# Kernel optimization log

Hardware: AMD Instinct MI355X
Metric: run time of the kernel (lower is better)

Reference implementation:

```python
import jax, jax.numpy as jnp
import numpy as np

N, D, H = 1024, 256, 256


def setup_inputs() -> dict:
    key = jax.random.key(0)
    k1, k2, k3, k4, k5 = jax.random.split(key, 5)
    z = jax.random.normal(k1, (N, D), dtype=jnp.float32)
    # fc1: Linear(2*D, H) -> weight [H, 2*D], bias [H]
    lim1 = 1.0 / np.sqrt(2 * D)
    W1 = jax.random.uniform(k2, (H, 2 * D), dtype=jnp.float32, minval=-lim1, maxval=lim1)
    b1 = jax.random.uniform(k3, (H,), dtype=jnp.float32, minval=-lim1, maxval=lim1)
    # fc2: Linear(H, 1)
    lim2 = 1.0 / np.sqrt(H)
    W2 = jax.random.uniform(k4, (1, H), dtype=jnp.float32, minval=-lim2, maxval=lim2)
    b2 = jax.random.uniform(k5, (1,), dtype=jnp.float32, minval=-lim2, maxval=lim2)
    return {"z": z, "W1": W1, "b1": b1, "W2": W2, "b2": b2}


def reference(z, W1, b1, W2, b2):
    # fc1 applied to concat([row, col]) splits algebraically:
    # cat(row, col) @ W1.T = row @ W1[:, :D].T + col @ W1[:, D:].T
    row_part = z @ W1[:, :D].T            # [N, H] (contribution of row element)
    col_part = z @ W1[:, D:].T            # [N, H] (contribution of col element)
    h = jax.nn.relu(row_part[:, None, :] + col_part[None, :, :] + b1)  # [N, N, H]
    out = jax.nn.sigmoid(jnp.einsum('ijh,h->ij', h, W2[0]) + b2[0])    # [N, N]
    return out
```

## Files before the change

kernel.cpp:

```cpp
#include <hip/hip_runtime.h>

#define NN 1024

typedef __attribute__((ext_vector_type(8))) short short8;
typedef __attribute__((ext_vector_type(4))) float floatx4;
typedef __attribute__((ext_vector_type(4))) unsigned int uint4v;
typedef _Float16 half2v __attribute__((ext_vector_type(2)));

#define R2_OFF   0u
#define CT_OFF   524288u

__device__ __forceinline__ unsigned short f2bf(float x) {
  unsigned u = __float_as_uint(x);
  return (unsigned short)((u + 0x7FFFu + ((u >> 16) & 1u)) >> 16);
}

__device__ __forceinline__ unsigned int pkf16(float a, float b) {
  unsigned int lo = (unsigned int)__builtin_bit_cast(unsigned short, (_Float16)a);
  unsigned int hi = (unsigned int)__builtin_bit_cast(unsigned short, (_Float16)b);
  return lo | (hi << 16);
}

__device__ __forceinline__ void dot2acc(unsigned int a, unsigned int b, float& acc) {
#if __has_builtin(__builtin_amdgcn_fdot2)
  acc = __builtin_amdgcn_fdot2(__builtin_bit_cast(half2v, a),
                               __builtin_bit_cast(half2v, b), acc, false);
#else
  asm("v_dot2_f32_f16 %0, %1, %2, %0" : "+v"(acc) : "v"(a), "v"(b));
#endif
}

__device__ __forceinline__ void pkmaxdot(unsigned int r, unsigned int c,
                                         unsigned int mul, float& acc) {
  unsigned int m;
  asm("v_pk_max_f16 %0, %1, %2" : "=v"(m) : "v"(r), "v"(c));
  dot2acc(m, mul, acc);
}

__global__ __launch_bounds__(256) void k1_fused(const float* __restrict__ z,
    const float* __restrict__ W1, const float* __restrict__ b1,
    const float* __restrict__ W2, char* __restrict__ ws) {
  __shared__ unsigned short zsh[16][272];
  __shared__ unsigned short wsh[4][16][272];
  __shared__ float tile[4][16][17];
  unsigned int* R2 = (unsigned int*)(ws + R2_OFF);
  unsigned int* Ct = (unsigned int*)(ws + CT_OFF);

  const int t = threadIdx.x;
  const int l = t & 63, w = t >> 6;
  const int i0 = blockIdx.x * 16;
  const int tid = blockIdx.y * 4 + w;
  const int q0 = tid * 16;
  const bool topR = q0 < 256;
  const int h0 = q0 & 255;
  const int off = topR ? 0 : 256;

  #pragma unroll
  for (int k = 0; k < 4; ++k) {
    const int f = t + k * 256;
    const int r = f >> 6, c4 = f & 63;
    const float4 v = *(const float4*)(z + (i0 + r) * 256 + c4 * 4);
    ushort4 u;
    u.x = f2bf(v.x); u.y = f2bf(v.y); u.z = f2bf(v.z); u.w = f2bf(v.w);
    *(ushort4*)&zsh[r][c4 * 4] = u;
  }
  #pragma unroll 4
  for (int r = 0; r < 16; ++r) {
    const int h = h0 + r;
    const float wa = fabsf(W2[h]);
    const float sc = topR ? wa : -wa;
    const float4 v = *(const float4*)(W1 + h * 512 + off + l * 4);
    ushort4 u;
    u.x = f2bf(v.x * sc); u.y = f2bf(v.y * sc);
    u.z = f2bf(v.z * sc); u.w = f2bf(v.w * sc);
    *(ushort4*)&wsh[w][r][l * 4] = u;
  }
  __syncthreads();

  floatx4 acc = {0.f, 0.f, 0.f, 0.f};
  const int fr = l & 15, fg = (l >> 4) * 8;
  #pragma unroll
  for (int kk = 0; kk < 8; ++kk) {
    const short8 a  = *(const short8*)&zsh[fr][fg + kk * 32];
    const short8 bb = *(const short8*)&wsh[w][fr][fg + kk * 32];
    acc = __builtin_amdgcn_mfma_f32_16x16x32_bf16(a, bb, acc, 0, 0, 0);
  }

  const int col = l & 15, r0 = (l >> 4) * 4;
  float bias = 0.f;
  if (topR) {
    const int h = q0 + col;
    bias = b1[h] * fabsf(W2[h]);
  }
  #pragma unroll
  for (int q = 0; q < 4; ++q) tile[w][r0 + q][col] = acc[q] + bias;
  __syncthreads();
  const int il = l & 15, g2 = l >> 4;
  if (topR) {
    #pragma unroll
    for (int e = 0; e < 2; ++e) {
      const int qc = g2 * 4 + e * 2;
      const unsigned int pk = pkf16(tile[w][il][qc], tile[w][il][qc + 1]);
      R2[((q0 >> 1) + g2 * 2 + e) * 1024 + (i0 + il)] = pk;
    }
  } else {
    const unsigned int pk0 = pkf16(tile[w][il][g2 * 4 + 0], tile[w][il][g2 * 4 + 1]);
    const unsigned int pk1 = pkf16(tile[w][il][g2 * 4 + 2], tile[w][il][g2 * 4 + 3]);
    const int hpg = ((q0 - 256) >> 3) + (g2 >> 1);
    unsigned int* dst = Ct + (hpg * 1024 + (i0 + il)) * 4 + (g2 & 1) * 2;
    dst[0] = pk0; dst[1] = pk1;
  }
}

__global__ __launch_bounds__(256) void k2_pair(const unsigned int* __restrict__ R2,
    const unsigned int* __restrict__ Ct, const float* __restrict__ W2,
    const float* __restrict__ b2v, float* __restrict__ out) {
  __shared__ unsigned int Rl[128][16];
  __shared__ unsigned int MulS[128];
  const int t = threadIdx.x;
  const int lane = t & 63, w = t >> 6;
  const int i0 = blockIdx.x * 16, j0 = blockIdx.y * 64;
  const int j = j0 + lane;

  if (t < 128) {
    const unsigned int s0 = (W2[2 * t]     > 0.f) ? 0x3C00u : 0xBC00u;
    const unsigned int s1 = (W2[2 * t + 1] > 0.f) ? 0x3C00u : 0xBC00u;
    MulS[t] = s0 | (s1 << 16);
  }
  #pragma unroll
  for (int k = 0; k < 8; ++k) {
    const int n = k * 256 + t;
    Rl[n >> 4][n & 15] = R2[(n >> 4) * 1024 + i0 + (n & 15)];
  }
  __syncthreads();

  const int iw = w * 4;
  float acc0 = 0.f, acc1 = 0.f, acc2 = 0.f, acc3 = 0.f, kv = 0.f;

  uint4v cc = *(const uint4v*)(Ct + j * 4);
  uint4v cn;
  #pragma unroll 2
  for (int g = 0; g < 32; ++g) {
    if (g < 31) cn = *(const uint4v*)(Ct + ((g + 1) * 1024 + j) * 4);
    const uint4v mq = *(const uint4v*)&MulS[g * 4];
    #pragma unroll
    for (int p = 0; p < 4; ++p) {
      const uint4v ra = *(const uint4v*)&Rl[g * 4 + p][iw];
      const unsigned int c = cc[p], mu = mq[p];
      dot2acc(c, mu, kv);
      pkmaxdot(ra[0], c, mu, acc0);
      pkmaxdot(ra[1], c, mu, acc1);
      pkmaxdot(ra[2], c, mu, acc2);
      pkmaxdot(ra[3], c, mu, acc3);
    }
    cc = cn;
  }

  const float base = b2v[0] - kv;
  out[(i0 + iw + 0) * NN + j] = 1.f / (1.f + __expf(-(acc0 + base)));
  out[(i0 + iw + 1) * NN + j] = 1.f / (1.f + __expf(-(acc1 + base)));
  out[(i0 + iw + 2) * NN + j] = 1.f / (1.f + __expf(-(acc2 + base)));
  out[(i0 + iw + 3) * NN + j] = 1.f / (1.f + __expf(-(acc3 + base)));
}

extern "C" void kernel_launch(void* const* d_in, const int* in_sizes, int n_in,
                              void* d_out, int out_size, void* d_ws, size_t ws_size,
                              hipStream_t stream) {
  const float* z  = (const float*)d_in[0];
  const float* W1 = (const float*)d_in[1];
  const float* b1 = (const float*)d_in[2];
  const float* W2 = (const float*)d_in[3];
  const float* b2 = (const float*)d_in[4];
  float* out = (float*)d_out;
  char* ws = (char*)d_ws;

  k1_fused<<<dim3(64, 8), 256, 0, stream>>>(z, W1, b1, W2, ws);
  k2_pair<<<dim3(64, 16), 256, 0, stream>>>(
      (const unsigned int*)(ws + R2_OFF), (const unsigned int*)(ws + CT_OFF),
      W2, b2, out);
}
```

Baseline: 26.18 us.

## Use f16 MFMA for the pairwise weighted reduction in the pair kernel

Rewrites the pair kernel so the per-(i,j) reduction over hidden units runs as an f16 MFMA: each lane computes packed max(R,C) fragments and feeds them as the A operand, with a broadcast sign vector as B. The kv term is computed separately per column and combined through shared memory. The aim is to move the dot2 reduction from VALU to matrix cores. In exchange it adds a 16-accumulator register footprint, scattered Ct loads and shared-memory staging of results. Most MFMA output columns are discarded, so much of the matrix throughput is wasted.

```diff
diff --git a/kernel.cpp b/kernel.cpp
--- a/kernel.cpp
+++ b/kernel.cpp
@@ -6,6 +6,7 @@
 typedef __attribute__((ext_vector_type(4))) float floatx4;
 typedef __attribute__((ext_vector_type(4))) unsigned int uint4v;
 typedef _Float16 half2v __attribute__((ext_vector_type(2)));
+typedef _Float16 half8 __attribute__((ext_vector_type(8)));
 
 #define R2_OFF   0u
 #define CT_OFF   524288u
@@ -28,13 +29,6 @@
 #else
   asm("v_dot2_f32_f16 %0, %1, %2, %0" : "+v"(acc) : "v"(a), "v"(b));
 #endif
-}
-
-__device__ __forceinline__ void pkmaxdot(unsigned int r, unsigned int c,
-                                         unsigned int mul, float& acc) {
-  unsigned int m;
-  asm("v_pk_max_f16 %0, %1, %2" : "=v"(m) : "v"(r), "v"(c));
-  dot2acc(m, mul, acc);
 }
 
 __global__ __launch_bounds__(256) void k1_fused(const float* __restrict__ z,
@@ -112,15 +106,16 @@
   }
 }
 
-__global__ __launch_bounds__(256) void k2_pair(const unsigned int* __restrict__ R2,
+__global__ __launch_bounds__(256) void k2_mfma(const unsigned int* __restrict__ R2,
     const unsigned int* __restrict__ Ct, const float* __restrict__ W2,
     const float* __restrict__ b2v, float* __restrict__ out) {
-  __shared__ unsigned int Rl[128][16];
+  __shared__ unsigned int Rl[16][144];
   __shared__ unsigned int MulS[128];
+  __shared__ float kvp[4][4][17];
+  __shared__ float ebuf[4][4][68];
   const int t = threadIdx.x;
-  const int lane = t & 63, w = t >> 6;
+  const int l = t & 63, w = t >> 6;
   const int i0 = blockIdx.x * 16, j0 = blockIdx.y * 64;
-  const int j = j0 + lane;
 
   if (t < 128) {
     const unsigned int s0 = (W2[2 * t]     > 0.f) ? 0x3C00u : 0xBC00u;
@@ -130,37 +125,65 @@
   #pragma unroll
   for (int k = 0; k < 8; ++k) {
     const int n = k * 256 + t;
-    Rl[n >> 4][n & 15] = R2[(n >> 4) * 1024 + i0 + (n & 15)];
-  }
-  __syncthreads();
-
-  const int iw = w * 4;
-  float acc0 = 0.f, acc1 = 0.f, acc2 = 0.f, acc3 = 0.f, kv = 0.f;
-
-  uint4v cc = *(const uint4v*)(Ct + j * 4);
-  uint4v cn;
-  #pragma unroll 2
-  for (int g = 0; g < 32; ++g) {
-    if (g < 31) cn = *(const uint4v*)(Ct + ((g + 1) * 1024 + j) * 4);
-    const uint4v mq = *(const uint4v*)&MulS[g * 4];
+    Rl[n & 15][n >> 4] = R2[(n >> 4) * 1024 + i0 + (n & 15)];
+  }
+  __syncthreads();
+
+  {
+    const int jj = l & 15, q = l >> 4;
+    float kp = 0.f;
     #pragma unroll
-    for (int p = 0; p < 4; ++p) {
-      const uint4v ra = *(const uint4v*)&Rl[g * 4 + p][iw];
-      const unsigned int c = cc[p], mu = mq[p];
-      dot2acc(c, mu, kv);
-      pkmaxdot(ra[0], c, mu, acc0);
-      pkmaxdot(ra[1], c, mu, acc1);
-      pkmaxdot(ra[2], c, mu, acc2);
-      pkmaxdot(ra[3], c, mu, acc3);
+    for (int gg = 0; gg < 8; ++gg) {
+      const int hpg = q * 8 + gg;
+      const uint4v cv = *(const uint4v*)(Ct + (hpg * 1024 + j0 + w * 16 + jj) * 4);
+      const uint4v mv = *(const uint4v*)&MulS[hpg * 4];
+      dot2acc(cv.x, mv.x, kp); dot2acc(cv.y, mv.y, kp);
+      dot2acc(cv.z, mv.z, kp); dot2acc(cv.w, mv.w, kp);
     }
-    cc = cn;
-  }
-
-  const float base = b2v[0] - kv;
-  out[(i0 + iw + 0) * NN + j] = 1.f / (1.f + __expf(-(acc0 + base)));
-  out[(i0 + iw + 1) * NN + j] = 1.f / (1.f + __expf(-(acc1 + base)));
-  out[(i0 + iw + 2) * NN + j] = 1.f / (1.f + __expf(-(acc2 + base)));
-  out[(i0 + iw + 3) * NN + j] = 1.f / (1.f + __expf(-(acc3 + base)));
+    kvp[w][q][jj] = kp;
+  }
+
+  const int kg = l >> 4;
+  const int iloc = (l & 15) >> 2;
+  const int jloc = l & 3;
+  const unsigned int* crow = Ct + (kg * 1024 + j0 + jloc) * 4;
+
+  floatx4 acc[16] = {};
+  #pragma unroll
+  for (int c = 0; c < 8; ++c) {
+    const uint4v Rf = *(const uint4v*)&Rl[w * 4 + iloc][c * 16 + kg * 4];
+    const uint4v Bf = *(const uint4v*)&MulS[c * 16 + kg * 4];
+    #pragma unroll
+    for (int g = 0; g < 16; ++g) {
+      const uint4v cv = *(const uint4v*)(crow + c * 16384 + g * 16);
+      unsigned int m0, m1, m2, m3;
+      asm("v_pk_max_f16 %0, %1, %2" : "=v"(m0) : "v"(Rf.x), "v"(cv.x));
+      asm("v_pk_max_f16 %0, %1, %2" : "=v"(m1) : "v"(Rf.y), "v"(cv.y));
+      asm("v_pk_max_f16 %0, %1, %2" : "=v"(m2) : "v"(Rf.z), "v"(cv.z));
+      asm("v_pk_max_f16 %0, %1, %2" : "=v"(m3) : "v"(Rf.w), "v"(cv.w));
+      uint4v av;
+      av.x = m0; av.y = m1; av.z = m2; av.w = m3;
+      acc[g] = __builtin_amdgcn_mfma_f32_16x16x32_f16(
+          __builtin_bit_cast(half8, av), __builtin_bit_cast(half8, Bf),
+          acc[g], 0, 0, 0);
+    }
+  }
+
+  #pragma unroll
+  for (int g = 0; g < 16; ++g) {
+    if ((l & 15) == g)
+      *(floatx4*)&ebuf[w][l >> 4][g * 4] = acc[g];
+  }
+  __syncthreads();
+
+  const int lw = l >> 4, jj = l & 15;
+  const float kvl = kvp[lw][0][jj] + kvp[lw][1][jj] + kvp[lw][2][jj] + kvp[lw][3][jj];
+  const float base = b2v[0] - kvl;
+  #pragma unroll
+  for (int s = 0; s < 4; ++s) {
+    const float x = ebuf[w][s][l] + base;
+    out[(i0 + w * 4 + s) * NN + j0 + l] = 1.f / (1.f + __expf(-x));
+  }
 }
 
 extern "C" void kernel_launch(void* const* d_in, const int* in_sizes, int n_in,
@@ -175,7 +198,7 @@
   char* ws = (char*)d_ws;
 
   k1_fused<<<dim3(64, 8), 256, 0, stream>>>(z, W1, b1, W2, ws);
-  k2_pair<<<dim3(64, 16), 256, 0, stream>>>(
+  k2_mfma<<<dim3(64, 16), 256, 0, stream>>>(
       (const unsigned int*)(ws + R2_OFF), (const unsigned int*)(ws + CT_OFF),
       W2, b2, out);
 }
```

Result: slower. 32.48 us (+24.1%).
